# Kernel tuning notes

Measured on AMD Instinct MI355X. Metric: run time of the kernel, lower is better.

The kernel has to match this reference:

```python
import jax, jax.numpy as jnp
import numpy as np

SHARED = 128  # matches TabularLoss(shared=128)


def _pairwise_dist(x, y):
    """Batched pairwise L2 distances. x: (B,N,D), y: (B,M,D) -> (B,N,M)."""
    sq = (jnp.sum(x * x, axis=-1)[:, :, None]
          + jnp.sum(y * y, axis=-1)[:, None, :]
          - 2.0 * jnp.einsum('bnd,bmd->bnm', x, y))
    sq = jnp.maximum(sq, 0.0)
    # safe sqrt (exact forward, no NaN grads at 0)
    return jnp.where(sq > 0, jnp.sqrt(jnp.where(sq > 0, sq, 1.0)), 0.0)


def _energy_distance(x, y):
    """geomloss SamplesLoss(loss='energy') with uniform weights.
    L = <a, D_xy b> - 0.5 <a, D_xx a> - 0.5 <b, D_yy b>, a=b=1/N.
    Returns per-batch losses, shape (B,)."""
    dxy = jnp.mean(_pairwise_dist(x, y), axis=(-2, -1))
    dxx = jnp.mean(_pairwise_dist(x, x), axis=(-2, -1))
    dyy = jnp.mean(_pairwise_dist(y, y), axis=(-2, -1))
    return dxy - 0.5 * dxx - 0.5 * dyy


def setup_inputs() -> dict:
    key = jax.random.key(0)
    k1, k2 = jax.random.split(key)
    total, genes = 8192, 5000
    return {
        'input': jax.random.normal(k1, (total, genes), dtype=jnp.float32),
        'target': jax.random.normal(k2, (total, genes), dtype=jnp.float32),
        'downsample': 64,
    }


def reference(input, target, downsample):
    x = input.reshape(-1, downsample, input.shape[-1])   # (B, N, G)
    y = target.reshape(-1, downsample, target.shape[-1])
    # gene-level MMD: each cell group is a point cloud of N cells in G dims
    gene_mmd = jnp.nanmean(_energy_distance(x, y))
    # cell-level MMD: transpose(2,0) -> (S, N, B): per shared gene, N points in B dims
    cx = jnp.transpose(x[:, :, -SHARED:], (2, 1, 0))
    cy = jnp.transpose(y[:, :, -SHARED:], (2, 1, 0))
    cell_mmd = jnp.nanmean(_energy_distance(cx, cy))
    loss = (jnp.where(jnp.isnan(gene_mmd), 0.0, gene_mmd)
            + jnp.where(jnp.isnan(cell_mmd), 0.0, cell_mmd))
    return loss
```

## Files before the change

### kernel.cpp

```cpp
#include <hip/hip_runtime.h>
#include <math.h>

#define TOTAL   8192
#define GENES   5000
#define NDS     64
#define NB      128
#define NSHARED 128
#define KC      64

#define GRAM_OFF 64

typedef __attribute__((ext_vector_type(8)))  short        short8;
typedef __attribute__((ext_vector_type(4)))  unsigned int uint4v;
typedef __attribute__((ext_vector_type(16))) float        f32x16;

typedef const __attribute__((address_space(1))) void* GPTR;
typedef __attribute__((address_space(3))) void*       LPTR;

#define GLOAD16(gp, lp) \
    __builtin_amdgcn_global_load_lds((GPTR)(gp), (LPTR)(lp), 16, 0, 0)

static __device__ inline unsigned int hpack2(float f0, float f1) {
    const unsigned int u0 = __builtin_bit_cast(unsigned int, f0) + 0x8000u;
    const unsigned int u1 = __builtin_bit_cast(unsigned int, f1) + 0x8000u;
    return (u1 & 0xFFFF0000u) | (u0 >> 16);
}
static __device__ inline short8 ldcvt_h(const float* base, int sw, int c0) {
    const float4 a = *(const float4*)(base + (((c0    ) ^ sw) << 2));
    const float4 b = *(const float4*)(base + (((c0 + 1) ^ sw) << 2));
    uint4v hv;
    hv[0] = hpack2(a.x, a.y); hv[1] = hpack2(a.z, a.w);
    hv[2] = hpack2(b.x, b.y); hv[3] = hpack2(b.z, b.w);
    return __builtin_bit_cast(short8, hv);
}

__global__ __launch_bounds__(256, 2)
void k_main(const float* __restrict__ X, const float* __restrict__ Y,
            const float* __restrict__ zsrc, float* __restrict__ grams,
            float* __restrict__ acc, int splitD, int Dper) {
    __shared__ __align__(16) float smem[16384];
    const int t = threadIdx.x;

    if ((int)blockIdx.x >= NSHARED) {
        const int blk = blockIdx.x - NSHARED;
        const int b = blk / splitD, c = blk % splitD;
        const int d0 = c * Dper;
        const int d1 = min(GENES, d0 + Dper);

        const float* __restrict__ xb = X + (size_t)b * NDS * GENES;
        const float* __restrict__ yb = Y + (size_t)b * NDS * GENES;

        float* sX = smem;
        float* sY = smem + 2 * NDS * KC;

        const int lane = t & 63;
        const int w    = t >> 6;
        const int qr   = w >> 1, qc = w & 1;
        const int lm   = lane & 31;
        const int kh2  = (lane >> 5) << 1;

        const int mr  = (qr << 5) + lm;
        const int mc  = (qc << 5) + lm;
        const int swr = mr & 15, swc = mc & 15;

        const int s16  = lane & 15;
        const int rsub = lane >> 4;
        const int rA = (w << 4) + rsub;
        const int rB = rA + 4, rC = rA + 8, rD = rA + 12;
        const int cA = (s16 ^ (rA & 15)) << 2;
        const int cB = (s16 ^ (rB & 15)) << 2;
        const int cC = (s16 ^ (rC & 15)) << 2;
        const int cD = (s16 ^ (rD & 15)) << 2;
        const float* gxA = xb + (size_t)rA * GENES + cA;
        const float* gxB = xb + (size_t)rB * GENES + cB;
        const float* gxC = xb + (size_t)rC * GENES + cC;
        const float* gxD = xb + (size_t)rD * GENES + cD;
        const float* gyA = yb + (size_t)rA * GENES + cA;
        const float* gyB = yb + (size_t)rB * GENES + cB;
        const float* gyC = yb + (size_t)rC * GENES + cC;
        const float* gyD = yb + (size_t)rD * GENES + cD;
        const int lA = ((w << 4) + 0) * KC;
        const int lB = lA + 4 * KC, lC = lA + 8 * KC, lD = lA + 12 * KC;

#define STAGEBUF(bofs, dd) do {                                               \
    const float* pxA = ((dd) + cA + 4 <= d1) ? gxA + (dd) : zsrc;             \
    const float* pxB = ((dd) + cB + 4 <= d1) ? gxB + (dd) : zsrc;             \
    const float* pxC = ((dd) + cC + 4 <= d1) ? gxC + (dd) : zsrc;             \
    const float* pxD = ((dd) + cD + 4 <= d1) ? gxD + (dd) : zsrc;             \
    const float* pyA = ((dd) + cA + 4 <= d1) ? gyA + (dd) : zsrc;             \
    const float* pyB = ((dd) + cB + 4 <= d1) ? gyB + (dd) : zsrc;             \
    const float* pyC = ((dd) + cC + 4 <= d1) ? gyC + (dd) : zsrc;             \
    const float* pyD = ((dd) + cD + 4 <= d1) ? gyD + (dd) : zsrc;             \
    GLOAD16(pxA, sX + (bofs) + lA);                                           \
    GLOAD16(pxB, sX + (bofs) + lB);                                           \
    GLOAD16(pxC, sX + (bofs) + lC);                                           \
    GLOAD16(pxD, sX + (bofs) + lD);                                           \
    GLOAD16(pyA, sY + (bofs) + lA);                                           \
    GLOAD16(pyB, sY + (bofs) + lB);                                           \
    GLOAD16(pyC, sY + (bofs) + lC);                                           \
    GLOAD16(pyD, sY + (bofs) + lD);                                           \
} while (0)

        f32x16 axy = {0,0,0,0,0,0,0,0,0,0,0,0,0,0,0,0};
        f32x16 axx = {0,0,0,0,0,0,0,0,0,0,0,0,0,0,0,0};
        f32x16 ayy = {0,0,0,0,0,0,0,0,0,0,0,0,0,0,0,0};

        const int nchunks = (d1 - d0 + KC - 1) / KC;

        STAGEBUF(0, d0);
        __syncthreads();

        for (int ci = 0; ci < nchunks; ++ci) {
            const int bofs = (ci & 1) * (NDS * KC);
            if (ci + 1 < nchunks)
                STAGEBUF(((ci + 1) & 1) * (NDS * KC), d0 + (ci + 1) * KC);

            const float* xrow = sX + bofs + mr * KC;
            const float* yrow = sY + bofs + mr * KC;
            const float* xcol = sX + bofs + mc * KC;
            const float* ycol = sY + bofs + mc * KC;
#pragma unroll
            for (int ks = 0; ks < 4; ++ks) {
                const int c0 = (ks << 2) + kh2;
                const short8 xr = ldcvt_h(xrow, swr, c0);
                const short8 yr = ldcvt_h(yrow, swr, c0);
                const short8 xc = ldcvt_h(xcol, swc, c0);
                const short8 yc = ldcvt_h(ycol, swc, c0);
                axy = __builtin_amdgcn_mfma_f32_32x32x16_bf16(xr, yc, axy, 0, 0, 0);
                axx = __builtin_amdgcn_mfma_f32_32x32x16_bf16(xr, xc, axx, 0, 0, 0);
                ayy = __builtin_amdgcn_mfma_f32_32x32x16_bf16(yr, yc, ayy, 0, 0, 0);
            }
            __syncthreads();
        }
#undef STAGEBUF

        float* g = grams + (size_t)(b * splitD + c) * 3 * 4096;
        const int col = (qc << 5) + lm;
#pragma unroll
        for (int r = 0; r < 16; ++r) {
            const int row = (qr << 5) + (r & 3) + ((r >> 2) << 3) + ((lane >> 5) << 2);
            g[0 * 4096 + row * 64 + col] = axy[r];
            g[1 * 4096 + row * 64 + col] = axx[r];
            g[2 * 4096 + row * 64 + col] = ayy[r];
        }
        return;
    }

    {
        const int s   = blockIdx.x;
        const int col = GENES - NSHARED + s;
        float* lds = smem;

#pragma unroll
        for (int k = 0; k < 32; ++k) {
            const int idx = t + 256 * k;
            lds[idx]        = X[(size_t)idx * GENES + col];
            lds[8192 + idx] = Y[(size_t)idx * GENES + col];
        }
        __syncthreads();

        const int ti = t & 15, tj = t >> 4;
        const int i0 = ti << 2, j0 = tj << 2;
        float axy[4][4] = {{0}}, axx[4][4] = {{0}}, ayy[4][4] = {{0}};

#pragma unroll 4
        for (int bb = 0; bb < NB; ++bb) {
            const float4 xi4 = *(const float4*)(lds + bb * 64 + i0);
            const float4 xj4 = *(const float4*)(lds + bb * 64 + j0);
            const float4 yi4 = *(const float4*)(lds + 8192 + bb * 64 + i0);
            const float4 yj4 = *(const float4*)(lds + 8192 + bb * 64 + j0);
            const float* xi = &xi4.x;
            const float* xj = &xj4.x;
            const float* yi = &yi4.x;
            const float* yj = &yj4.x;
#pragma unroll
            for (int ii = 0; ii < 4; ++ii) {
#pragma unroll
                for (int jj = 0; jj < 4; ++jj) {
                    axy[ii][jj] = fmaf(xi[ii], yj[jj], axy[ii][jj]);
                    axx[ii][jj] = fmaf(xi[ii], xj[jj], axx[ii][jj]);
                    ayy[ii][jj] = fmaf(yi[ii], yj[jj], ayy[ii][jj]);
                }
            }
        }
        __syncthreads();
#pragma unroll
        for (int ii = 0; ii < 4; ++ii) {
            float4 v;
            v.x = axy[ii][0]; v.y = axy[ii][1]; v.z = axy[ii][2]; v.w = axy[ii][3];
            *(float4*)(lds + 0 * 4096 + (i0 + ii) * 64 + j0) = v;
            v.x = axx[ii][0]; v.y = axx[ii][1]; v.z = axx[ii][2]; v.w = axx[ii][3];
            *(float4*)(lds + 1 * 4096 + (i0 + ii) * 64 + j0) = v;
            v.x = ayy[ii][0]; v.y = ayy[ii][1]; v.z = ayy[ii][2]; v.w = ayy[ii][3];
            *(float4*)(lds + 2 * 4096 + (i0 + ii) * 64 + j0) = v;
        }
        __syncthreads();

        float local = 0.f;
#pragma unroll
        for (int k = 0; k < 16; ++k) {
            const int e = t + 256 * k;
            const int i = e >> 6, j = e & 63;
            const float gxy = lds[e];
            const float gxx = lds[4096 + e];
            const float gyy = lds[8192 + e];
            const float nxi = lds[4096 + i * 65], nxj = lds[4096 + j * 65];
            const float nyi = lds[8192 + i * 65], nyj = lds[8192 + j * 65];
            const float dxy = sqrtf(fmaxf(nxi + nyj - 2.f * gxy, 0.f));
            const float dxx = sqrtf(fmaxf(nxi + nxj - 2.f * gxx, 0.f));
            const float dyy = sqrtf(fmaxf(nyi + nyj - 2.f * gyy, 0.f));
            local += dxy - 0.5f * (dxx + dyy);
        }
#pragma unroll
        for (int off = 32; off; off >>= 1) local += __shfl_down(local, off);
        __syncthreads();
        if ((t & 63) == 0) lds[t >> 6] = local;
        __syncthreads();
        if (t == 0) {
            const float bl = lds[0] + lds[1] + lds[2] + lds[3];
            atomicAdd(acc + 1, bl * (1.0f / (4096.0f * (float)NSHARED)));
        }
    }
}

__global__ __launch_bounds__(256) void k_gene_dist(const float* __restrict__ grams,
                                                   float* __restrict__ acc,
                                                   int splitD) {
    const int b = blockIdx.x, t = threadIdx.x;
    __shared__ __align__(16) float G[3 * 4096];
    __shared__ float red[4];

    for (int m = 0; m < 3; ++m) {
#pragma unroll
        for (int k = 0; k < 16; ++k) {
            const int e = t + 256 * k;
            float s = 0.f;
            for (int c = 0; c < splitD; ++c)
                s += grams[((size_t)(b * splitD + c) * 3 + m) * 4096 + e];
            G[m * 4096 + e] = s;
        }
    }
    __syncthreads();

    float local = 0.f;
#pragma unroll
    for (int k = 0; k < 16; ++k) {
        const int e = t + 256 * k;
        const int i = e >> 6, j = e & 63;
        const float gxy = G[e];
        const float gxx = G[4096 + e];
        const float gyy = G[8192 + e];
        const float nxi = G[4096 + i * 65], nxj = G[4096 + j * 65];
        const float nyi = G[8192 + i * 65], nyj = G[8192 + j * 65];
        const float dxy = sqrtf(fmaxf(nxi + nyj - 2.f * gxy, 0.f));
        const float dxx = sqrtf(fmaxf(nxi + nxj - 2.f * gxx, 0.f));
        const float dyy = sqrtf(fmaxf(nyi + nyj - 2.f * gyy, 0.f));
        local += dxy - 0.5f * (dxx + dyy);
    }
#pragma unroll
    for (int off = 32; off; off >>= 1) local += __shfl_down(local, off);
    if ((t & 63) == 0) red[t >> 6] = local;
    __syncthreads();
    if (t == 0) {
        const float bl = red[0] + red[1] + red[2] + red[3];
        atomicAdd(acc, bl * (1.0f / (4096.0f * (float)NB)));
    }
}

__global__ void k_final(const float* __restrict__ acc, float* __restrict__ out) {
    out[0] = acc[0] + acc[1];
}

extern "C" void kernel_launch(void* const* d_in, const int* in_sizes, int n_in,
                              void* d_out, int out_size, void* d_ws, size_t ws_size,
                              hipStream_t stream) {
    const float* X = (const float*)d_in[0];
    const float* Y = (const float*)d_in[1];
    float* out = (float*)d_out;
    float* ws  = (float*)d_ws;

    int splitD = 4;
    while (splitD > 1 &&
           ((size_t)GRAM_OFF + (size_t)splitD * NB * 3 * 4096) * sizeof(float) > ws_size)
        splitD >>= 1;
    const int chunks = (GENES + KC - 1) / KC;
    const int cper   = (chunks + splitD - 1) / splitD;
    const int Dper   = cper * KC;

    float* acc   = ws;
    float* zsrc  = ws + 32;
    float* grams = ws + GRAM_OFF;

    hipMemsetAsync(ws, 0, GRAM_OFF * sizeof(float), stream);
    hipLaunchKernelGGL(k_main, dim3(NSHARED + NB * splitD), dim3(256), 0, stream,
                       X, Y, zsrc, grams, acc, splitD, Dper);
    hipLaunchKernelGGL(k_gene_dist, dim3(NB), dim3(256), 0, stream,
                       grams, acc + 0, splitD);
    hipLaunchKernelGGL(k_final, dim3(1), dim3(1), 0, stream, acc, out);
}
```

Baseline: 160.2 us.

## Fuse gene-distance and final kernels into main via last-block atomic counters

The per-batch gram reduction and distance computation, plus the final sum, move into k_main. For each batch, the last finishing split-D block is found with an atomic counter and does the reduction. A global done counter then lets the very last block write the output. This removes two extra kernel launches and the gaps between them, at the cost of thread fences, atomics and a serial tail on the last block of each batch.

```diff
diff --git a/kernel.cpp b/kernel.cpp
--- a/kernel.cpp
+++ b/kernel.cpp
@@ -8,7 +8,7 @@
 #define NSHARED 128
 #define KC      64
 
-#define GRAM_OFF 64
+#define GRAM_OFF 256
 
 typedef __attribute__((ext_vector_type(8)))  short        short8;
 typedef __attribute__((ext_vector_type(4)))  unsigned int uint4v;
@@ -37,8 +37,11 @@
 __global__ __launch_bounds__(256, 2)
 void k_main(const float* __restrict__ X, const float* __restrict__ Y,
             const float* __restrict__ zsrc, float* __restrict__ grams,
-            float* __restrict__ acc, int splitD, int Dper) {
+            float* __restrict__ acc, int* __restrict__ cnt,
+            int* __restrict__ done, float* __restrict__ out,
+            int splitD, int Dper) {
     __shared__ __align__(16) float smem[16384];
+    __shared__ int isLast;
     const int t = threadIdx.x;
 
     if ((int)blockIdx.x >= NSHARED) {
@@ -143,6 +146,64 @@
             g[1 * 4096 + row * 64 + col] = axx[r];
             g[2 * 4096 + row * 64 + col] = ayy[r];
         }
+
+        __threadfence();
+        __syncthreads();
+        if (t == 0) {
+            const int old = __hip_atomic_fetch_add(&cnt[b], 1,
+                                __ATOMIC_ACQ_REL, __HIP_MEMORY_SCOPE_AGENT);
+            isLast = (old == splitD - 1);
+        }
+        __syncthreads();
+        if (!isLast) return;
+
+        float* G = smem;
+        for (int m = 0; m < 3; ++m) {
+#pragma unroll
+            for (int k = 0; k < 16; ++k) {
+                const int e = t + 256 * k;
+                float s = 0.f;
+                for (int cc = 0; cc < splitD; ++cc)
+                    s += grams[((size_t)(b * splitD + cc) * 3 + m) * 4096 + e];
+                G[m * 4096 + e] = s;
+            }
+        }
+        __syncthreads();
+
+        float local = 0.f;
+#pragma unroll
+        for (int k = 0; k < 16; ++k) {
+            const int e = t + 256 * k;
+            const int i = e >> 6, j = e & 63;
+            const float gxy = G[e];
+            const float gxx = G[4096 + e];
+            const float gyy = G[8192 + e];
+            const float nxi = G[4096 + i * 65], nxj = G[4096 + j * 65];
+            const float nyi = G[8192 + i * 65], nyj = G[8192 + j * 65];
+            const float dxy = sqrtf(fmaxf(nxi + nyj - 2.f * gxy, 0.f));
+            const float dxx = sqrtf(fmaxf(nxi + nxj - 2.f * gxx, 0.f));
+            const float dyy = sqrtf(fmaxf(nyi + nyj - 2.f * gyy, 0.f));
+            local += dxy - 0.5f * (dxx + dyy);
+        }
+#pragma unroll
+        for (int off = 32; off; off >>= 1) local += __shfl_down(local, off);
+        float* red = smem + 12288;
+        if ((t & 63) == 0) red[t >> 6] = local;
+        __syncthreads();
+        if (t == 0) {
+            const float bl = red[0] + red[1] + red[2] + red[3];
+            atomicAdd(acc, bl * (1.0f / (4096.0f * (float)NB)));
+            __threadfence();
+            const int old = __hip_atomic_fetch_add(done, 1,
+                                __ATOMIC_ACQ_REL, __HIP_MEMORY_SCOPE_AGENT);
+            if (old == NB + NSHARED - 1) {
+                const float a0 = __hip_atomic_load(acc,
+                                    __ATOMIC_RELAXED, __HIP_MEMORY_SCOPE_AGENT);
+                const float a1 = __hip_atomic_load(acc + 1,
+                                    __ATOMIC_RELAXED, __HIP_MEMORY_SCOPE_AGENT);
+                out[0] = a0 + a1;
+            }
+        }
         return;
     }
 
@@ -219,56 +280,18 @@
         if (t == 0) {
             const float bl = lds[0] + lds[1] + lds[2] + lds[3];
             atomicAdd(acc + 1, bl * (1.0f / (4096.0f * (float)NSHARED)));
+            __threadfence();
+            const int old = __hip_atomic_fetch_add(done, 1,
+                                __ATOMIC_ACQ_REL, __HIP_MEMORY_SCOPE_AGENT);
+            if (old == NB + NSHARED - 1) {
+                const float a0 = __hip_atomic_load(acc,
+                                    __ATOMIC_RELAXED, __HIP_MEMORY_SCOPE_AGENT);
+                const float a1 = __hip_atomic_load(acc + 1,
+                                    __ATOMIC_RELAXED, __HIP_MEMORY_SCOPE_AGENT);
+                out[0] = a0 + a1;
+            }
         }
     }
-}
-
-__global__ __launch_bounds__(256) void k_gene_dist(const float* __restrict__ grams,
-                                                   float* __restrict__ acc,
-                                                   int splitD) {
-    const int b = blockIdx.x, t = threadIdx.x;
-    __shared__ __align__(16) float G[3 * 4096];
-    __shared__ float red[4];
-
-    for (int m = 0; m < 3; ++m) {
-#pragma unroll
-        for (int k = 0; k < 16; ++k) {
-            const int e = t + 256 * k;
-            float s = 0.f;
-            for (int c = 0; c < splitD; ++c)
-                s += grams[((size_t)(b * splitD + c) * 3 + m) * 4096 + e];
-            G[m * 4096 + e] = s;
-        }
-    }
-    __syncthreads();
-
-    float local = 0.f;
-#pragma unroll
-    for (int k = 0; k < 16; ++k) {
-        const int e = t + 256 * k;
-        const int i = e >> 6, j = e & 63;
-        const float gxy = G[e];
-        const float gxx = G[4096 + e];
-        const float gyy = G[8192 + e];
-        const float nxi = G[4096 + i * 65], nxj = G[4096 + j * 65];
-        const float nyi = G[8192 + i * 65], nyj = G[8192 + j * 65];
-        const float dxy = sqrtf(fmaxf(nxi + nyj - 2.f * gxy, 0.f));
-        const float dxx = sqrtf(fmaxf(nxi + nxj - 2.f * gxx, 0.f));
-        const float dyy = sqrtf(fmaxf(nyi + nyj - 2.f * gyy, 0.f));
-        local += dxy - 0.5f * (dxx + dyy);
-    }
-#pragma unroll
-    for (int off = 32; off; off >>= 1) local += __shfl_down(local, off);
-    if ((t & 63) == 0) red[t >> 6] = local;
-    __syncthreads();
-    if (t == 0) {
-        const float bl = red[0] + red[1] + red[2] + red[3];
-        atomicAdd(acc, bl * (1.0f / (4096.0f * (float)NB)));
-    }
-}
-
-__global__ void k_final(const float* __restrict__ acc, float* __restrict__ out) {
-    out[0] = acc[0] + acc[1];
 }
 
 extern "C" void kernel_launch(void* const* d_in, const int* in_sizes, int n_in,
@@ -289,12 +312,11 @@
 
     float* acc   = ws;
     float* zsrc  = ws + 32;
+    int*   cnt   = (int*)(ws + 64);
+    int*   done  = (int*)(ws + 192);
     float* grams = ws + GRAM_OFF;
 
     hipMemsetAsync(ws, 0, GRAM_OFF * sizeof(float), stream);
     hipLaunchKernelGGL(k_main, dim3(NSHARED + NB * splitD), dim3(256), 0, stream,
-                       X, Y, zsrc, grams, acc, splitD, Dper);
-    hipLaunchKernelGGL(k_gene_dist, dim3(NB), dim3(256), 0, stream,
-                       grams, acc + 0, splitD);
-    hipLaunchKernelGGL(k_final, dim3(1), dim3(1), 0, stream, acc, out);
+                       X, Y, zsrc, grams, acc, cnt, done, out, splitD, Dper);
 }
```

Result: slower. 286.0 us (+78.6%).

## Replace syncthreads double-buffer loop with explicit vmcnt-waited ping-pong pipeline

Applied to the files above, without the earlier changes.

Rewrites the Gram-matrix main loop as an unrolled two-buffer ping-pong with compile-time LDS offsets. Explicit s_waitcnt vmcnt(8) lets the next chunk's global-to-LDS loads stay in flight while only the current chunk is waited on. Raw s_barrier and sched_barrier calls replace __syncthreads. This is meant to overlap memory loads with MFMA work more tightly and drop redundant full waits. It relies on hand-written waitcnt counts matching the eight loads issued per stage, which is fragile.

```diff
diff --git a/kernel.cpp b/kernel.cpp
--- a/kernel.cpp
+++ b/kernel.cpp
@@ -49,9 +49,6 @@
 
         const float* __restrict__ xb = X + (size_t)b * NDS * GENES;
         const float* __restrict__ yb = Y + (size_t)b * NDS * GENES;
-
-        float* sX = smem;
-        float* sY = smem + 2 * NDS * KC;
 
         const int lane = t & 63;
         const int w    = t >> 6;
@@ -82,7 +79,7 @@
         const int lA = ((w << 4) + 0) * KC;
         const int lB = lA + 4 * KC, lC = lA + 8 * KC, lD = lA + 12 * KC;
 
-#define STAGEBUF(bofs, dd) do {                                               \
+#define STAGE(SX, SY, dd) do {                                                \
     const float* pxA = ((dd) + cA + 4 <= d1) ? gxA + (dd) : zsrc;             \
     const float* pxB = ((dd) + cB + 4 <= d1) ? gxB + (dd) : zsrc;             \
     const float* pxC = ((dd) + cC + 4 <= d1) ? gxC + (dd) : zsrc;             \
@@ -91,15 +88,42 @@
     const float* pyB = ((dd) + cB + 4 <= d1) ? gyB + (dd) : zsrc;             \
     const float* pyC = ((dd) + cC + 4 <= d1) ? gyC + (dd) : zsrc;             \
     const float* pyD = ((dd) + cD + 4 <= d1) ? gyD + (dd) : zsrc;             \
-    GLOAD16(pxA, sX + (bofs) + lA);                                           \
-    GLOAD16(pxB, sX + (bofs) + lB);                                           \
-    GLOAD16(pxC, sX + (bofs) + lC);                                           \
-    GLOAD16(pxD, sX + (bofs) + lD);                                           \
-    GLOAD16(pyA, sY + (bofs) + lA);                                           \
-    GLOAD16(pyB, sY + (bofs) + lB);                                           \
-    GLOAD16(pyC, sY + (bofs) + lC);                                           \
-    GLOAD16(pyD, sY + (bofs) + lD);                                           \
+    GLOAD16(pxA, (SX) + lA);                                                  \
+    GLOAD16(pxB, (SX) + lB);                                                  \
+    GLOAD16(pxC, (SX) + lC);                                                  \
+    GLOAD16(pxD, (SX) + lD);                                                  \
+    GLOAD16(pyA, (SY) + lA);                                                  \
+    GLOAD16(pyB, (SY) + lB);                                                  \
+    GLOAD16(pyC, (SY) + lC);                                                  \
+    GLOAD16(pyD, (SY) + lD);                                                  \
 } while (0)
+
+#define COMPUTE(SX, SY) do {                                                  \
+    const float* xrow = (SX) + mr * KC;                                       \
+    const float* yrow = (SY) + mr * KC;                                       \
+    const float* xcol = (SX) + mc * KC;                                       \
+    const float* ycol = (SY) + mc * KC;                                       \
+    _Pragma("unroll")                                                         \
+    for (int ks = 0; ks < 4; ++ks) {                                          \
+        const int c0 = (ks << 2) + kh2;                                       \
+        const short8 xr = ldcvt_h(xrow, swr, c0);                             \
+        const short8 yr = ldcvt_h(yrow, swr, c0);                             \
+        const short8 xc = ldcvt_h(xcol, swc, c0);                             \
+        const short8 yc = ldcvt_h(ycol, swc, c0);                             \
+        axy = __builtin_amdgcn_mfma_f32_32x32x16_bf16(xr, yc, axy, 0, 0, 0);  \
+        axx = __builtin_amdgcn_mfma_f32_32x32x16_bf16(xr, xc, axx, 0, 0, 0);  \
+        ayy = __builtin_amdgcn_mfma_f32_32x32x16_bf16(yr, yc, ayy, 0, 0, 0);  \
+    }                                                                         \
+} while (0)
+
+#define VM8  do { asm volatile("s_waitcnt vmcnt(8)" ::: "memory");            \
+                  __builtin_amdgcn_sched_barrier(0); } while (0)
+#define VM0  do { asm volatile("s_waitcnt vmcnt(0)" ::: "memory");            \
+                  __builtin_amdgcn_sched_barrier(0); } while (0)
+#define LGKM do { asm volatile("s_waitcnt lgkmcnt(0)" ::: "memory");          \
+                  __builtin_amdgcn_sched_barrier(0); } while (0)
+#define BAR  do { __builtin_amdgcn_s_barrier();                               \
+                  __builtin_amdgcn_sched_barrier(0); } while (0)
 
         f32x16 axy = {0,0,0,0,0,0,0,0,0,0,0,0,0,0,0,0};
         f32x16 axx = {0,0,0,0,0,0,0,0,0,0,0,0,0,0,0,0};
@@ -107,32 +131,43 @@
 
         const int nchunks = (d1 - d0 + KC - 1) / KC;
 
-        STAGEBUF(0, d0);
-        __syncthreads();
-
-        for (int ci = 0; ci < nchunks; ++ci) {
-            const int bofs = (ci & 1) * (NDS * KC);
-            if (ci + 1 < nchunks)
-                STAGEBUF(((ci + 1) & 1) * (NDS * KC), d0 + (ci + 1) * KC);
-
-            const float* xrow = sX + bofs + mr * KC;
-            const float* yrow = sY + bofs + mr * KC;
-            const float* xcol = sX + bofs + mc * KC;
-            const float* ycol = sY + bofs + mc * KC;
-#pragma unroll
-            for (int ks = 0; ks < 4; ++ks) {
-                const int c0 = (ks << 2) + kh2;
-                const short8 xr = ldcvt_h(xrow, swr, c0);
-                const short8 yr = ldcvt_h(yrow, swr, c0);
-                const short8 xc = ldcvt_h(xcol, swc, c0);
-                const short8 yc = ldcvt_h(ycol, swc, c0);
-                axy = __builtin_amdgcn_mfma_f32_32x32x16_bf16(xr, yc, axy, 0, 0, 0);
-                axx = __builtin_amdgcn_mfma_f32_32x32x16_bf16(xr, xc, axx, 0, 0, 0);
-                ayy = __builtin_amdgcn_mfma_f32_32x32x16_bf16(yr, yc, ayy, 0, 0, 0);
+        STAGE(smem, smem + 8192, d0);
+        __builtin_amdgcn_sched_barrier(0);
+
+        int ci = 0;
+        while (true) {
+            if (ci + 1 < nchunks) {
+                STAGE(smem + 4096, smem + 12288, d0 + (ci + 1) * KC);
+                __builtin_amdgcn_sched_barrier(0);
+                VM8;
+            } else {
+                VM0;
             }
-            __syncthreads();
-        }
-#undef STAGEBUF
+            BAR;
+            COMPUTE(smem, smem + 8192);
+            LGKM;
+            BAR;
+            if (++ci >= nchunks) break;
+
+            if (ci + 1 < nchunks) {
+                STAGE(smem, smem + 8192, d0 + (ci + 1) * KC);
+                __builtin_amdgcn_sched_barrier(0);
+                VM8;
+            } else {
+                VM0;
+            }
+            BAR;
+            COMPUTE(smem + 4096, smem + 12288);
+            LGKM;
+            BAR;
+            if (++ci >= nchunks) break;
+        }
+#undef STAGE
+#undef COMPUTE
+#undef VM8
+#undef VM0
+#undef LGKM
+#undef BAR
 
         float* g = grams + (size_t)(b * splitD + c) * 3 * 4096;
         const int col = (qc << 5) + lm;
```

Measured after the change: 160.9 us. No clear change (+0.4%).

## Give each wave private LDS tiles and drop block-wide barriers in gram loop

Applied to the files above, without the earlier changes.

Each wave now stages only the row blocks it needs for its own 32x32 output quadrant into a private LDS region, with KC reduced to 32. This removes the double-buffered shared staging and the per-chunk __syncthreads, replacing them with per-wave waitcnt on vmcnt and lgkmcnt. Cross-wave prefetch overlap is lost: loads are issued and then waited on immediately each chunk. Off-diagonal waves load twice the data, so global and LDS traffic per block rises.

```diff
diff --git a/kernel.cpp b/kernel.cpp
--- a/kernel.cpp
+++ b/kernel.cpp
@@ -6,7 +6,7 @@
 #define NDS     64
 #define NB      128
 #define NSHARED 128
-#define KC      64
+#define KC      32
 
 #define GRAM_OFF 64
 
@@ -50,55 +50,38 @@
         const float* __restrict__ xb = X + (size_t)b * NDS * GENES;
         const float* __restrict__ yb = Y + (size_t)b * NDS * GENES;
 
-        float* sX = smem;
-        float* sY = smem + 2 * NDS * KC;
-
         const int lane = t & 63;
         const int w    = t >> 6;
         const int qr   = w >> 1, qc = w & 1;
         const int lm   = lane & 31;
-        const int kh2  = (lane >> 5) << 1;
-
-        const int mr  = (qr << 5) + lm;
-        const int mc  = (qc << 5) + lm;
-        const int swr = mr & 15, swc = mc & 15;
-
-        const int s16  = lane & 15;
-        const int rsub = lane >> 4;
-        const int rA = (w << 4) + rsub;
-        const int rB = rA + 4, rC = rA + 8, rD = rA + 12;
-        const int cA = (s16 ^ (rA & 15)) << 2;
-        const int cB = (s16 ^ (rB & 15)) << 2;
-        const int cC = (s16 ^ (rC & 15)) << 2;
-        const int cD = (s16 ^ (rD & 15)) << 2;
-        const float* gxA = xb + (size_t)rA * GENES + cA;
-        const float* gxB = xb + (size_t)rB * GENES + cB;
-        const float* gxC = xb + (size_t)rC * GENES + cC;
-        const float* gxD = xb + (size_t)rD * GENES + cD;
-        const float* gyA = yb + (size_t)rA * GENES + cA;
-        const float* gyB = yb + (size_t)rB * GENES + cB;
-        const float* gyC = yb + (size_t)rC * GENES + cC;
-        const float* gyD = yb + (size_t)rD * GENES + cD;
-        const int lA = ((w << 4) + 0) * KC;
-        const int lB = lA + 4 * KC, lC = lA + 8 * KC, lD = lA + 12 * KC;
-
-#define STAGEBUF(bofs, dd) do {                                               \
-    const float* pxA = ((dd) + cA + 4 <= d1) ? gxA + (dd) : zsrc;             \
-    const float* pxB = ((dd) + cB + 4 <= d1) ? gxB + (dd) : zsrc;             \
-    const float* pxC = ((dd) + cC + 4 <= d1) ? gxC + (dd) : zsrc;             \
-    const float* pxD = ((dd) + cD + 4 <= d1) ? gxD + (dd) : zsrc;             \
-    const float* pyA = ((dd) + cA + 4 <= d1) ? gyA + (dd) : zsrc;             \
-    const float* pyB = ((dd) + cB + 4 <= d1) ? gyB + (dd) : zsrc;             \
-    const float* pyC = ((dd) + cC + 4 <= d1) ? gyC + (dd) : zsrc;             \
-    const float* pyD = ((dd) + cD + 4 <= d1) ? gyD + (dd) : zsrc;             \
-    GLOAD16(pxA, sX + (bofs) + lA);                                           \
-    GLOAD16(pxB, sX + (bofs) + lB);                                           \
-    GLOAD16(pxC, sX + (bofs) + lC);                                           \
-    GLOAD16(pxD, sX + (bofs) + lD);                                           \
-    GLOAD16(pyA, sY + (bofs) + lA);                                           \
-    GLOAD16(pyB, sY + (bofs) + lB);                                           \
-    GLOAD16(pyC, sY + (bofs) + lC);                                           \
-    GLOAD16(pyD, sY + (bofs) + lD);                                           \
+        const int kh   = lane >> 5;
+        const bool diag = (qr == qc);
+
+        float* XA = smem + (w << 12);
+        float* XB = diag ? XA : (XA + 1024);
+        float* YA = XA + 2048;
+        float* YB = diag ? YA : (XA + 3072);
+
+        const int lr = lane >> 3;
+        const int gb = (lane & 7) ^ lr;
+        const int gofs = gb << 2;
+        const int rowA = (qr << 5) + lr;
+        const int rowB = (qc << 5) + lr;
+        const float* xA = xb + (size_t)rowA * GENES + gofs;
+        const float* yA = yb + (size_t)rowA * GENES + gofs;
+        const float* xB = xb + (size_t)rowB * GENES + gofs;
+        const float* yB = yb + (size_t)rowB * GENES + gofs;
+
+#define STAGE_SET(BUF, P, dd) do {                                           \
+    const int okv = ((dd) + gofs + 4 <= d1);                                 \
+    const float* p0 = okv ? (P) + (dd)                  : zsrc;              \
+    const float* p1 = okv ? (P) + (dd) +  8 * GENES     : zsrc;              \
+    const float* p2 = okv ? (P) + (dd) + 16 * GENES     : zsrc;              \
+    const float* p3 = okv ? (P) + (dd) + 24 * GENES     : zsrc;              \
+    GLOAD16(p0, (BUF));                                                      \
+    GLOAD16(p1, (BUF) + 256);                                                \
+    GLOAD16(p2, (BUF) + 512);                                                \
+    GLOAD16(p3, (BUF) + 768);                                                \
 } while (0)
 
         f32x16 axy = {0,0,0,0,0,0,0,0,0,0,0,0,0,0,0,0};
@@ -106,33 +89,40 @@
         f32x16 ayy = {0,0,0,0,0,0,0,0,0,0,0,0,0,0,0,0};
 
         const int nchunks = (d1 - d0 + KC - 1) / KC;
-
-        STAGEBUF(0, d0);
-        __syncthreads();
+        const int sw = lm & 7;
+        const float* rXA = XA + lm * KC;
+        const float* rXB = XB + lm * KC;
+        const float* rYA = YA + lm * KC;
+        const float* rYB = YB + lm * KC;
 
         for (int ci = 0; ci < nchunks; ++ci) {
-            const int bofs = (ci & 1) * (NDS * KC);
-            if (ci + 1 < nchunks)
-                STAGEBUF(((ci + 1) & 1) * (NDS * KC), d0 + (ci + 1) * KC);
-
-            const float* xrow = sX + bofs + mr * KC;
-            const float* yrow = sY + bofs + mr * KC;
-            const float* xcol = sX + bofs + mc * KC;
-            const float* ycol = sY + bofs + mc * KC;
-#pragma unroll
-            for (int ks = 0; ks < 4; ++ks) {
-                const int c0 = (ks << 2) + kh2;
-                const short8 xr = ldcvt_h(xrow, swr, c0);
-                const short8 yr = ldcvt_h(yrow, swr, c0);
-                const short8 xc = ldcvt_h(xcol, swc, c0);
-                const short8 yc = ldcvt_h(ycol, swc, c0);
-                axy = __builtin_amdgcn_mfma_f32_32x32x16_bf16(xr, yc, axy, 0, 0, 0);
-                axx = __builtin_amdgcn_mfma_f32_32x32x16_bf16(xr, xc, axx, 0, 0, 0);
-                ayy = __builtin_amdgcn_mfma_f32_32x32x16_bf16(yr, yc, ayy, 0, 0, 0);
+            const int dd = d0 + ci * KC;
+            STAGE_SET(XA, xA, dd);
+            STAGE_SET(YA, yA, dd);
+            if (!diag) {
+                STAGE_SET(XA + 1024, xB, dd);
+                STAGE_SET(XA + 3072, yB, dd);
             }
-            __syncthreads();
-        }
-#undef STAGEBUF
+            __builtin_amdgcn_sched_barrier(0);
+            asm volatile("s_waitcnt vmcnt(0)" ::: "memory");
+            __builtin_amdgcn_sched_barrier(0);
+
+#pragma unroll
+            for (int ks = 0; ks < 2; ++ks) {
+                const int c0 = (ks << 2) + (kh << 1);
+                const short8 xa = ldcvt_h(rXA, sw, c0);
+                const short8 ya = ldcvt_h(rYA, sw, c0);
+                const short8 xc = ldcvt_h(rXB, sw, c0);
+                const short8 yc = ldcvt_h(rYB, sw, c0);
+                axy = __builtin_amdgcn_mfma_f32_32x32x16_bf16(xa, yc, axy, 0, 0, 0);
+                axx = __builtin_amdgcn_mfma_f32_32x32x16_bf16(xa, xc, axx, 0, 0, 0);
+                ayy = __builtin_amdgcn_mfma_f32_32x32x16_bf16(ya, yc, ayy, 0, 0, 0);
+            }
+            __builtin_amdgcn_sched_barrier(0);
+            asm volatile("s_waitcnt lgkmcnt(0)" ::: "memory");
+            __builtin_amdgcn_sched_barrier(0);
+        }
+#undef STAGE_SET
 
         float* g = grams + (size_t)(b * splitD + c) * 3 * 4096;
         const int col = (qc << 5) + lm;
```

Result: slower. 216.0 us (+34.8%).
